# Kernel tuning notes

Hardware: AMD Instinct MI355X
Metric: run time of the kernel (lower is better)

## Reference

```python
import jax, jax.numpy as jnp
import numpy as np

B, D, S = 16, 512, 1500   # batch, input_size, seq_len
E, K, L = 8, 1024, 8      # embedding_size, num_embeddings, num_layers
TAU = 1.0
EPS = 1e-12               # F.normalize default eps


def setup_inputs() -> dict:
    key = jax.random.key(0)
    ks = jax.random.split(key, 5)
    x = jax.random.normal(ks[0], (B, D, S), dtype=jnp.float32)
    # weight-norm parametrized 1x1 conv params (v direction, g magnitude, bias)
    in_v = jax.random.normal(ks[1], (L, E, D), dtype=jnp.float32) * 0.05
    in_g = jnp.ones((L, E), dtype=jnp.float32)
    in_b = jnp.zeros((L, E), dtype=jnp.float32)
    out_v = jax.random.normal(ks[2], (L, D, E), dtype=jnp.float32) * 0.05
    out_g = jnp.ones((L, D), dtype=jnp.float32)
    out_b = jnp.zeros((L, D), dtype=jnp.float32)
    codebook = jax.random.normal(ks[3], (L, K, E), dtype=jnp.float32)
    return dict(x=x, in_v=in_v, in_g=in_g, in_b=in_b,
                out_v=out_v, out_g=out_g, out_b=out_b, codebook=codebook)


def _wn(v, g):
    # torch weight_norm (dim=0): w = g * v / ||v|| with norm over all dims except out-channel
    n = jnp.sqrt(jnp.sum(v * v, axis=1, keepdims=True))
    return g[:, None] * v / n


def _l2norm(x):
    # F.normalize(p=2, eps=1e-12)
    n = jnp.linalg.norm(x, axis=-1, keepdims=True)
    return x / jnp.maximum(n, EPS)


def _vq_layer(xr, iv, ig, ib, ov, og, ob, cb):
    Wi = _wn(iv, ig)                                              # [E, D]
    x_proj = jnp.einsum('ed,bds->bes', Wi, xr) + ib[:, None]      # [B, E, S]
    xf = x_proj.transpose(0, 2, 1).reshape(B * S, E)              # [B*S, E]
    xn = _l2norm(xf)
    cn = _l2norm(cb)                                              # [K, E]
    dist = (jnp.sum(xn * xn, axis=1, keepdims=True)
            - 2.0 * (xn @ cn.T)
            + jnp.sum(cn * cn, axis=1)[None, :])                  # [B*S, K]
    logits = -dist / TAU
    idxs = jnp.argmax(-dist, axis=1).reshape(B, S)                # [B, S]
    xq = cb[idxs].transpose(0, 2, 1)                              # [B, E, S] (un-normalized codebook)
    commit = jnp.mean((x_proj - jax.lax.stop_gradient(xq)) ** 2, axis=(1, 2))  # per-batch
    cbloss = jnp.mean((xq - jax.lax.stop_gradient(x_proj)) ** 2, axis=(1, 2))
    xq_st = x_proj + jax.lax.stop_gradient(xq - x_proj)           # straight-through
    Wo = _wn(ov, og)                                              # [D, E]
    xq_out = jnp.einsum('de,bes->bds', Wo, xq_st) + ob[:, None]   # [B, D, S]
    return xq_out, logits, idxs, commit, cbloss


def reference(x, in_v, in_g, in_b, out_v, out_g, out_b, codebook):
    # eval mode: all layers active, mask all-ones => masked mean == plain batch mean
    xq_sum = jnp.zeros_like(x)
    xr = x
    idxs_l, logits_l = [], []
    commit = jnp.float32(0.0)
    cbl = jnp.float32(0.0)
    for i in range(L):
        xq, lg, ix, cl, bl = _vq_layer(xr, in_v[i], in_g[i], in_b[i],
                                       out_v[i], out_g[i], out_b[i], codebook[i])
        xq_sum = xq_sum + xq
        xr = xr - xq
        commit = commit + jnp.mean(cl)
        cbl = cbl + jnp.mean(bl)
        idxs_l.append(ix)
        logits_l.append(lg)
    x_idxs = jnp.stack(idxs_l, axis=1)     # [B, L, S]
    x_logits = jnp.stack(logits_l, axis=1) # [B*S, L, K]
    return xq_sum, x_idxs, x_logits, commit, cbl
```

## Files before the change

### kernel.cpp

```cpp
#include <hip/hip_runtime.h>

constexpr int Lx = 8;
constexpr int Bx = 16;
constexpr int Dx = 512;
constexpr int Sx = 1500;
constexpr int Ex = 8;
constexpr int Kx = 1024;
constexpr int BS = Bx * Sx;
#define EPSF 1e-12f

__global__ __launch_bounds__(64) void k_wn_in(const float* __restrict__ v,
                                              const float* __restrict__ g,
                                              float* __restrict__ Wi) {
    int row = blockIdx.x;
    int lane = threadIdx.x;
    const float* vr = v + row * Dx;
    float s = 0.f;
    for (int j = lane; j < Dx; j += 64) { float t = vr[j]; s += t * t; }
    for (int off = 32; off; off >>= 1) s += __shfl_down(s, off);
    s = __shfl(s, 0);
    float scale = g[row] / sqrtf(s);
    for (int j = lane; j < Dx; j += 64) Wi[row * Dx + j] = vr[j] * scale;
}

__global__ __launch_bounds__(256) void k_wn_out_cb(const float* __restrict__ ov,
                                                   const float* __restrict__ og,
                                                   const float* __restrict__ cb,
                                                   float* __restrict__ Wo,
                                                   float* __restrict__ cn,
                                                   float* __restrict__ cc) {
    int r = blockIdx.x * blockDim.x + threadIdx.x;
    if (r < Lx * Dx) {
        const float* vr = ov + r * Ex;
        float s = 0.f;
        for (int e = 0; e < Ex; e++) s += vr[e] * vr[e];
        float sc = og[r] / sqrtf(s);
        for (int e = 0; e < Ex; e++) Wo[r * Ex + e] = vr[e] * sc;
    } else {
        int q = r - Lx * Dx;
        if (q < Lx * Kx) {
            const float* vr = cb + q * Ex;
            float s = 0.f;
            for (int e = 0; e < Ex; e++) s += vr[e] * vr[e];
            float n = fmaxf(sqrtf(s), EPSF);
            float s2 = 0.f, qv[Ex];
            for (int e = 0; e < Ex; e++) { qv[e] = vr[e] / n; s2 += qv[e] * qv[e]; }
            for (int e = 0; e < Ex; e++) cn[q * Ex + e] = qv[e];
            cc[q] = s2;
        }
    }
}


__global__ __launch_bounds__(256) void k_copyx(const float4* __restrict__ x,
                                               float4* __restrict__ xr,
                                               double* __restrict__ acc, unsigned n4) {
    unsigned i = blockIdx.x * blockDim.x + threadIdx.x;
    if (i == 0) *acc = 0.0;
    for (; i < n4; i += gridDim.x * blockDim.x) xr[i] = x[i];
}

__global__ __launch_bounds__(256) void k_proj(const float* __restrict__ xr,
                                              const float* __restrict__ Wi,
                                              const float* __restrict__ ib,
                                              float* __restrict__ xproj, int l) {
    __shared__ float wi[Ex * Dx];
    __shared__ float red[4 * Ex * 64];
    const float* W = Wi + l * Ex * Dx;
    for (int i = threadIdx.x; i < Ex * Dx; i += 256) wi[i] = W[i];
    __syncthreads();
    int col = threadIdx.x & 63;
    int grp = threadIdx.x >> 6;
    int c = blockIdx.x * 64 + col;
    int b = c / Sx, s = c % Sx;
    const float* xrb = xr + (size_t)b * Dx * Sx + s;
    float acc[Ex] = {0, 0, 0, 0, 0, 0, 0, 0};
    for (int d = grp * 128; d < grp * 128 + 128; d++) {
        float v = xrb[(size_t)d * Sx];
        #pragma unroll
        for (int e = 0; e < Ex; e++) acc[e] += wi[e * Dx + d] * v;
    }
    #pragma unroll
    for (int e = 0; e < Ex; e++) red[(grp * Ex + e) * 64 + col] = acc[e];
    __syncthreads();
    for (int o = threadIdx.x; o < Ex * 64; o += 256) {
        int e = o >> 6, cl = o & 63;
        float sum = red[(0 * Ex + e) * 64 + cl] + red[(1 * Ex + e) * 64 + cl] +
                    red[(2 * Ex + e) * 64 + cl] + red[(3 * Ex + e) * 64 + cl];
        int c2 = blockIdx.x * 64 + cl;
        int b2 = c2 / Sx, s2 = c2 % Sx;
        xproj[((size_t)b2 * Ex + e) * Sx + s2] = sum + ib[l * Ex + e];
    }
}

__global__ __launch_bounds__(256) void k_vq(const float* __restrict__ xproj,
                                            const float* __restrict__ cn,
                                            const float* __restrict__ cc,
                                            const float* __restrict__ cb,
                                            float* __restrict__ logits,
                                            float* __restrict__ idxs,
                                            float* __restrict__ xq,
                                            double* __restrict__ acc, int l) {
    __shared__ float4 cnt4[Kx * 2];
    __shared__ float  ccs[Kx];
    __shared__ float  bred[4];
    const float4* cn4 = (const float4*)(cn + (size_t)l * Kx * Ex);
    for (int i = threadIdx.x; i < Kx * 2; i += 256)
        cnt4[i ^ ((i >> 3) & 1)] = cn4[i];
    for (int i = threadIdx.x; i < Kx; i += 256) ccs[i] = cc[l * Kx + i];
    __syncthreads();
    int wave = threadIdx.x >> 6, lane = threadIdx.x & 63;
    float lossp = 0.f;
    for (int rr = 0; rr < 4; rr++) {
        int c = blockIdx.x * 16 + wave * 4 + rr;
        int b = c / Sx, s = c % Sx;
        float xp[Ex]; float xx2 = 0.f;
        #pragma unroll
        for (int e = 0; e < Ex; e++) {
            xp[e] = xproj[((size_t)b * Ex + e) * Sx + s];
            xx2 += xp[e] * xp[e];
        }
        float nrm = fmaxf(sqrtf(xx2), EPSF);
        float xn[Ex]; float xx = 0.f;
        #pragma unroll
        for (int e = 0; e < Ex; e++) { xn[e] = xp[e] / nrm; xx += xn[e] * xn[e]; }
        float* lrow = logits + ((size_t)c * Lx + l) * Kx;
        float best = -3.0e38f; int bk = 0;
        for (int j = 0; j < 16; j++) {
            int k = j * 64 + lane;
            float4 c0 = cnt4[(k * 2 + 0) ^ ((k >> 2) & 1)];
            float4 c1 = cnt4[(k * 2 + 1) ^ ((k >> 2) & 1)];
            float dot = xn[0] * c0.x + xn[1] * c0.y + xn[2] * c0.z + xn[3] * c0.w +
                        xn[4] * c1.x + xn[5] * c1.y + xn[6] * c1.z + xn[7] * c1.w;
            float lg = -(xx - 2.f * dot + ccs[k]);
            lrow[k] = lg;
            if (lg > best) { best = lg; bk = k; }
        }
        for (int off = 32; off; off >>= 1) {
            float ov = __shfl_xor(best, off);
            int   oi = __shfl_xor(bk, off);
            if (ov > best || (ov == best && oi < bk)) { best = ov; bk = oi; }
        }
        if (lane == 0) idxs[((size_t)b * Lx + l) * Sx + s] = (float)bk;
        const float* cbe = cb + ((size_t)l * Kx + bk) * Ex;
        if (lane < Ex) {
            float q = cbe[lane];
            xq[((size_t)b * Ex + lane) * Sx + s] = q;
            float dl = xp[lane] - q;
            lossp += dl * dl;
        }
    }
    for (int off = 32; off; off >>= 1) lossp += __shfl_down(lossp, off);
    if (lane == 0) bred[wave] = lossp;
    __syncthreads();
    if (threadIdx.x == 0) {
        float t = bred[0] + bred[1] + bred[2] + bred[3];
        atomicAdd(acc, (double)t);
    }
}

__global__ __launch_bounds__(256) void k_outproj(float* __restrict__ xr,
                                                 const float* __restrict__ xq,
                                                 const float* __restrict__ Wo,
                                                 const float* __restrict__ ob, int l) {
    const float* W   = Wo + l * Dx * Ex;
    const float* obl = ob + l * Dx;
    const unsigned S4 = Sx / 4;
    const unsigned n4 = Bx * Dx * S4;
    for (unsigned i = blockIdx.x * blockDim.x + threadIdx.x; i < n4;
         i += gridDim.x * blockDim.x) {
        unsigned s4 = i % S4;
        unsigned bd = i / S4;
        unsigned d = bd % Dx;
        unsigned b = bd / Dx;
        float4 av = {0, 0, 0, 0};
        #pragma unroll
        for (int e = 0; e < Ex; e++) {
            float w = W[d * Ex + e];
            float4 q = *(const float4*)(xq + ((size_t)b * Ex + e) * Sx + s4 * 4);
            av.x += w * q.x; av.y += w * q.y; av.z += w * q.z; av.w += w * q.w;
        }
        float bias = obl[d];
        float4 r = *(const float4*)(xr + (size_t)bd * Sx + s4 * 4);
        r.x -= av.x + bias; r.y -= av.y + bias;
        r.z -= av.z + bias; r.w -= av.w + bias;
        *(float4*)(xr + (size_t)bd * Sx + s4 * 4) = r;
    }
}

__global__ __launch_bounds__(256) void k_final(const float4* __restrict__ x,
                                               float4* __restrict__ out0,
                                               const double* __restrict__ acc,
                                               float* __restrict__ commit,
                                               float* __restrict__ cbl, unsigned n4) {
    unsigned i = blockIdx.x * blockDim.x + threadIdx.x;
    if (i == 0) {
        float v = (float)(*acc / (double)(Bx * Ex * Sx));
        *commit = v;
        *cbl = v;
    }
    for (; i < n4; i += gridDim.x * blockDim.x) {
        float4 a = x[i], b = out0[i];
        float4 o = {a.x - b.x, a.y - b.y, a.z - b.z, a.w - b.w};
        out0[i] = o;
    }
}

extern "C" void kernel_launch(void* const* d_in, const int* in_sizes, int n_in,
                              void* d_out, int out_size, void* d_ws, size_t ws_size,
                              hipStream_t stream) {
    const float* x     = (const float*)d_in[0];
    const float* in_v  = (const float*)d_in[1];
    const float* in_g  = (const float*)d_in[2];
    const float* in_b  = (const float*)d_in[3];
    const float* out_v = (const float*)d_in[4];
    const float* out_g = (const float*)d_in[5];
    const float* out_b = (const float*)d_in[6];
    const float* cb    = (const float*)d_in[7];

    float* out = (float*)d_out;
    float* xr       = out;
    float* oidx     = out + 12288000;
    float* ologits  = out + 12480000;
    float* ocommit  = out + 209088000;
    float* ocbl     = out + 209088001;

    char* w = (char*)d_ws;
    float*  Wi    = (float*)(w);
    float*  Wo    = (float*)(w + 131072);
    float*  cn    = (float*)(w + 262144);
    float*  cc    = (float*)(w + 524288);
    float*  xproj = (float*)(w + 557056);
    float*  xq    = (float*)(w + 1325056);
    double* acc   = (double*)(w + 2093056);

    k_wn_in<<<Lx * Ex, 64, 0, stream>>>(in_v, in_g, Wi);
    k_wn_out_cb<<<(Lx * Dx + Lx * Kx) / 256, 256, 0, stream>>>(out_v, out_g, cb, Wo, cn, cc);
    k_copyx<<<2048, 256, 0, stream>>>((const float4*)x, (float4*)xr, acc, 3072000u);

    for (int l = 0; l < Lx; l++) {
        k_proj<<<BS / 64, 256, 0, stream>>>(xr, Wi, in_b, xproj, l);
        k_vq<<<BS / 16, 256, 0, stream>>>(xproj, cn, cc, cb, ologits, oidx, xq, acc, l);
        k_outproj<<<2048, 256, 0, stream>>>(xr, xq, Wo, out_b, l);
    }
    k_final<<<2048, 256, 0, stream>>>((const float4*)x, (float4*)xr, acc,
                                      ocommit, ocbl, 3072000u);
}
```

Measured before the change: 760.8 us.

## Fuse all VQ layers into one register-resident megakernel per column tile

Replaces the per-layer projection, VQ and output-projection kernels with a single kernel in which each block holds 32 sequence columns of the residual (512 channels) in registers across all 8 layers. The residual is never written back to global memory between layers, which removes the repeated full-tensor reads and writes along with the copy and final kernels. The input weights are transposed so they can be read as float4. Holding 64 floats of residual per thread raises register pressure and the grid is smaller (750 blocks). The logits write stays the dominant traffic.

```diff
diff --git a/kernel.cpp b/kernel.cpp
--- a/kernel.cpp
+++ b/kernel.cpp
@@ -11,8 +11,9 @@
 
 __global__ __launch_bounds__(64) void k_wn_in(const float* __restrict__ v,
                                               const float* __restrict__ g,
-                                              float* __restrict__ Wi) {
+                                              float* __restrict__ WiT) {
     int row = blockIdx.x;
+    int l = row >> 3, e = row & 7;
     int lane = threadIdx.x;
     const float* vr = v + row * Dx;
     float s = 0.f;
@@ -20,7 +21,8 @@
     for (int off = 32; off; off >>= 1) s += __shfl_down(s, off);
     s = __shfl(s, 0);
     float scale = g[row] / sqrtf(s);
-    for (int j = lane; j < Dx; j += 64) Wi[row * Dx + j] = vr[j] * scale;
+    for (int j = lane; j < Dx; j += 64)
+        WiT[((size_t)l * Dx + j) * Ex + e] = vr[j] * scale;
 }
 
 __global__ __launch_bounds__(256) void k_wn_out_cb(const float* __restrict__ ov,
@@ -28,181 +30,180 @@
                                                    const float* __restrict__ cb,
                                                    float* __restrict__ Wo,
                                                    float* __restrict__ cn,
-                                                   float* __restrict__ cc) {
+                                                   float* __restrict__ cc,
+                                                   double* __restrict__ acc) {
     int r = blockIdx.x * blockDim.x + threadIdx.x;
+    if (r == 0) *acc = 0.0;
     if (r < Lx * Dx) {
         const float* vr = ov + r * Ex;
         float s = 0.f;
+        #pragma unroll
         for (int e = 0; e < Ex; e++) s += vr[e] * vr[e];
         float sc = og[r] / sqrtf(s);
+        #pragma unroll
         for (int e = 0; e < Ex; e++) Wo[r * Ex + e] = vr[e] * sc;
     } else {
         int q = r - Lx * Dx;
         if (q < Lx * Kx) {
             const float* vr = cb + q * Ex;
             float s = 0.f;
+            #pragma unroll
             for (int e = 0; e < Ex; e++) s += vr[e] * vr[e];
             float n = fmaxf(sqrtf(s), EPSF);
             float s2 = 0.f, qv[Ex];
+            #pragma unroll
             for (int e = 0; e < Ex; e++) { qv[e] = vr[e] / n; s2 += qv[e] * qv[e]; }
+            #pragma unroll
             for (int e = 0; e < Ex; e++) cn[q * Ex + e] = qv[e];
             cc[q] = s2;
         }
     }
 }
 
-
-__global__ __launch_bounds__(256) void k_copyx(const float4* __restrict__ x,
-                                               float4* __restrict__ xr,
-                                               double* __restrict__ acc, unsigned n4) {
-    unsigned i = blockIdx.x * blockDim.x + threadIdx.x;
-    if (i == 0) *acc = 0.0;
-    for (; i < n4; i += gridDim.x * blockDim.x) xr[i] = x[i];
-}
-
-__global__ __launch_bounds__(256) void k_proj(const float* __restrict__ xr,
-                                              const float* __restrict__ Wi,
-                                              const float* __restrict__ ib,
-                                              float* __restrict__ xproj, int l) {
-    __shared__ float wi[Ex * Dx];
-    __shared__ float red[4 * Ex * 64];
-    const float* W = Wi + l * Ex * Dx;
-    for (int i = threadIdx.x; i < Ex * Dx; i += 256) wi[i] = W[i];
-    __syncthreads();
-    int col = threadIdx.x & 63;
-    int grp = threadIdx.x >> 6;
-    int c = blockIdx.x * 64 + col;
-    int b = c / Sx, s = c % Sx;
-    const float* xrb = xr + (size_t)b * Dx * Sx + s;
-    float acc[Ex] = {0, 0, 0, 0, 0, 0, 0, 0};
-    for (int d = grp * 128; d < grp * 128 + 128; d++) {
-        float v = xrb[(size_t)d * Sx];
-        #pragma unroll
-        for (int e = 0; e < Ex; e++) acc[e] += wi[e * Dx + d] * v;
-    }
-    #pragma unroll
-    for (int e = 0; e < Ex; e++) red[(grp * Ex + e) * 64 + col] = acc[e];
-    __syncthreads();
-    for (int o = threadIdx.x; o < Ex * 64; o += 256) {
-        int e = o >> 6, cl = o & 63;
-        float sum = red[(0 * Ex + e) * 64 + cl] + red[(1 * Ex + e) * 64 + cl] +
-                    red[(2 * Ex + e) * 64 + cl] + red[(3 * Ex + e) * 64 + cl];
-        int c2 = blockIdx.x * 64 + cl;
-        int b2 = c2 / Sx, s2 = c2 % Sx;
-        xproj[((size_t)b2 * Ex + e) * Sx + s2] = sum + ib[l * Ex + e];
-    }
-}
-
-__global__ __launch_bounds__(256) void k_vq(const float* __restrict__ xproj,
-                                            const float* __restrict__ cn,
-                                            const float* __restrict__ cc,
-                                            const float* __restrict__ cb,
-                                            float* __restrict__ logits,
-                                            float* __restrict__ idxs,
-                                            float* __restrict__ xq,
-                                            double* __restrict__ acc, int l) {
+__global__ __launch_bounds__(256, 2) void k_mega(const float* __restrict__ x,
+                                                 const float* __restrict__ WiT,
+                                                 const float* __restrict__ ibias,
+                                                 const float* __restrict__ Wo,
+                                                 const float* __restrict__ obias,
+                                                 const float* __restrict__ cb,
+                                                 const float* __restrict__ cn,
+                                                 const float* __restrict__ cc,
+                                                 float* __restrict__ out0,
+                                                 float* __restrict__ oidx,
+                                                 float* __restrict__ logits,
+                                                 double* __restrict__ acc) {
     __shared__ float4 cnt4[Kx * 2];
     __shared__ float  ccs[Kx];
+    __shared__ float  red[8 * Ex * 32];
+    __shared__ float  xprojs[Ex * 32];
+    __shared__ float  xqs[Ex * 32];
     __shared__ float  bred[4];
-    const float4* cn4 = (const float4*)(cn + (size_t)l * Kx * Ex);
-    for (int i = threadIdx.x; i < Kx * 2; i += 256)
-        cnt4[i ^ ((i >> 3) & 1)] = cn4[i];
-    for (int i = threadIdx.x; i < Kx; i += 256) ccs[i] = cc[l * Kx + i];
-    __syncthreads();
-    int wave = threadIdx.x >> 6, lane = threadIdx.x & 63;
+
+    const int t = threadIdx.x;
+    const int col = t & 31;
+    const int g = t >> 5;
+    const int wave = t >> 6, lane = t & 63;
+    const int c = blockIdx.x * 32 + col;
+    const int b = c / Sx;
+    const int s = c - b * Sx;
+    const float* xcol = x + (size_t)b * Dx * Sx + s;
+
+    float xr[64];
+    #pragma unroll
+    for (int i = 0; i < 64; i++) xr[i] = xcol[(size_t)(g * 64 + i) * Sx];
+
     float lossp = 0.f;
-    for (int rr = 0; rr < 4; rr++) {
-        int c = blockIdx.x * 16 + wave * 4 + rr;
-        int b = c / Sx, s = c % Sx;
-        float xp[Ex]; float xx2 = 0.f;
-        #pragma unroll
-        for (int e = 0; e < Ex; e++) {
-            xp[e] = xproj[((size_t)b * Ex + e) * Sx + s];
-            xx2 += xp[e] * xp[e];
-        }
-        float nrm = fmaxf(sqrtf(xx2), EPSF);
-        float xn[Ex]; float xx = 0.f;
-        #pragma unroll
-        for (int e = 0; e < Ex; e++) { xn[e] = xp[e] / nrm; xx += xn[e] * xn[e]; }
-        float* lrow = logits + ((size_t)c * Lx + l) * Kx;
-        float best = -3.0e38f; int bk = 0;
-        for (int j = 0; j < 16; j++) {
-            int k = j * 64 + lane;
-            float4 c0 = cnt4[(k * 2 + 0) ^ ((k >> 2) & 1)];
-            float4 c1 = cnt4[(k * 2 + 1) ^ ((k >> 2) & 1)];
-            float dot = xn[0] * c0.x + xn[1] * c0.y + xn[2] * c0.z + xn[3] * c0.w +
-                        xn[4] * c1.x + xn[5] * c1.y + xn[6] * c1.z + xn[7] * c1.w;
-            float lg = -(xx - 2.f * dot + ccs[k]);
-            lrow[k] = lg;
-            if (lg > best) { best = lg; bk = k; }
-        }
-        for (int off = 32; off; off >>= 1) {
-            float ov = __shfl_xor(best, off);
-            int   oi = __shfl_xor(bk, off);
-            if (ov > best || (ov == best && oi < bk)) { best = ov; bk = oi; }
-        }
-        if (lane == 0) idxs[((size_t)b * Lx + l) * Sx + s] = (float)bk;
-        const float* cbe = cb + ((size_t)l * Kx + bk) * Ex;
-        if (lane < Ex) {
-            float q = cbe[lane];
-            xq[((size_t)b * Ex + lane) * Sx + s] = q;
-            float dl = xp[lane] - q;
-            lossp += dl * dl;
-        }
-    }
+
+    for (int l = 0; l < Lx; l++) {
+        const float4* cn4 = (const float4*)(cn + (size_t)l * Kx * Ex);
+        for (int i2 = t; i2 < Kx * 2; i2 += 256)
+            cnt4[i2 ^ ((i2 >> 3) & 1)] = cn4[i2];
+        for (int i2 = t; i2 < Kx; i2 += 256) ccs[i2] = cc[l * Kx + i2];
+        __syncthreads();
+
+        const float4* wt = (const float4*)(WiT + (size_t)l * Dx * Ex);
+        float pacc[8] = {0, 0, 0, 0, 0, 0, 0, 0};
+        #pragma unroll
+        for (int i = 0; i < 64; i++) {
+            int d = g * 64 + i;
+            float4 w0 = wt[d * 2 + 0];
+            float4 w1 = wt[d * 2 + 1];
+            float v = xr[i];
+            pacc[0] += w0.x * v; pacc[1] += w0.y * v;
+            pacc[2] += w0.z * v; pacc[3] += w0.w * v;
+            pacc[4] += w1.x * v; pacc[5] += w1.y * v;
+            pacc[6] += w1.z * v; pacc[7] += w1.w * v;
+        }
+        #pragma unroll
+        for (int e = 0; e < 8; e++) red[(g * 8 + e) * 32 + col] = pacc[e];
+        __syncthreads();
+
+        {
+            float sum = 0.f;
+            #pragma unroll
+            for (int gg = 0; gg < 8; gg++) sum += red[(gg * 8 + g) * 32 + col];
+            xprojs[g * 32 + col] = sum + ibias[l * Ex + g];
+        }
+        __syncthreads();
+
+        for (int cl = 0; cl < 8; cl++) {
+            int mycol = wave * 8 + cl;
+            int mc = blockIdx.x * 32 + mycol;
+            int mb = mc / Sx, ms = mc - mb * Sx;
+            float xp[8]; float xx2 = 0.f;
+            #pragma unroll
+            for (int e = 0; e < 8; e++) {
+                xp[e] = xprojs[e * 32 + mycol];
+                xx2 += xp[e] * xp[e];
+            }
+            float nrm = fmaxf(sqrtf(xx2), EPSF);
+            float xn[8]; float xx = 0.f;
+            #pragma unroll
+            for (int e = 0; e < 8; e++) { xn[e] = xp[e] / nrm; xx += xn[e] * xn[e]; }
+            float* lrow = logits + ((size_t)mc * Lx + l) * Kx;
+            float best = -3.0e38f; int bk = 0;
+            for (int j = 0; j < 16; j++) {
+                int k = j * 64 + lane;
+                float4 c0 = cnt4[(k * 2 + 0) ^ ((k >> 2) & 1)];
+                float4 c1 = cnt4[(k * 2 + 1) ^ ((k >> 2) & 1)];
+                float dot = xn[0] * c0.x + xn[1] * c0.y + xn[2] * c0.z + xn[3] * c0.w +
+                            xn[4] * c1.x + xn[5] * c1.y + xn[6] * c1.z + xn[7] * c1.w;
+                float lg = -(xx - 2.f * dot + ccs[k]);
+                lrow[k] = lg;
+                if (lg > best) { best = lg; bk = k; }
+            }
+            for (int off = 32; off; off >>= 1) {
+                float ov = __shfl_xor(best, off);
+                int   oi = __shfl_xor(bk, off);
+                if (ov > best || (ov == best && oi < bk)) { best = ov; bk = oi; }
+            }
+            if (lane == 0) oidx[((size_t)mb * Lx + l) * Sx + ms] = (float)bk;
+            if (lane < 8) {
+                float q = cb[((size_t)l * Kx + bk) * Ex + lane];
+                xqs[lane * 32 + mycol] = q;
+                float dl = xprojs[lane * 32 + mycol] - q;
+                lossp += dl * dl;
+            }
+        }
+        __syncthreads();
+
+        float xq[8];
+        #pragma unroll
+        for (int e = 0; e < 8; e++) xq[e] = xqs[e * 32 + col];
+        const float4* wo4 = (const float4*)(Wo + (size_t)l * Dx * Ex);
+        const float* obl = obias + l * Dx;
+        #pragma unroll
+        for (int i = 0; i < 64; i++) {
+            int d = g * 64 + i;
+            float4 w0 = wo4[d * 2 + 0];
+            float4 w1 = wo4[d * 2 + 1];
+            float dsum = w0.x * xq[0] + w0.y * xq[1] + w0.z * xq[2] + w0.w * xq[3] +
+                         w1.x * xq[4] + w1.y * xq[5] + w1.z * xq[6] + w1.w * xq[7] +
+                         obl[d];
+            xr[i] -= dsum;
+        }
+    }
+
+    float* ocol = out0 + (size_t)b * Dx * Sx + s;
+    #pragma unroll
+    for (int i = 0; i < 64; i++) {
+        float xv = xcol[(size_t)(g * 64 + i) * Sx];
+        ocol[(size_t)(g * 64 + i) * Sx] = xv - xr[i];
+    }
+
     for (int off = 32; off; off >>= 1) lossp += __shfl_down(lossp, off);
     if (lane == 0) bred[wave] = lossp;
     __syncthreads();
+    if (t == 0)
+        atomicAdd(acc, (double)(bred[0] + bred[1] + bred[2] + bred[3]));
+}
+
+__global__ void k_scalar(const double* __restrict__ acc,
+                         float* __restrict__ commit, float* __restrict__ cbl) {
     if (threadIdx.x == 0) {
-        float t = bred[0] + bred[1] + bred[2] + bred[3];
-        atomicAdd(acc, (double)t);
-    }
-}
-
-__global__ __launch_bounds__(256) void k_outproj(float* __restrict__ xr,
-                                                 const float* __restrict__ xq,
-                                                 const float* __restrict__ Wo,
-                                                 const float* __restrict__ ob, int l) {
-    const float* W   = Wo + l * Dx * Ex;
-    const float* obl = ob + l * Dx;
-    const unsigned S4 = Sx / 4;
-    const unsigned n4 = Bx * Dx * S4;
-    for (unsigned i = blockIdx.x * blockDim.x + threadIdx.x; i < n4;
-         i += gridDim.x * blockDim.x) {
-        unsigned s4 = i % S4;
-        unsigned bd = i / S4;
-        unsigned d = bd % Dx;
-        unsigned b = bd / Dx;
-        float4 av = {0, 0, 0, 0};
-        #pragma unroll
-        for (int e = 0; e < Ex; e++) {
-            float w = W[d * Ex + e];
-            float4 q = *(const float4*)(xq + ((size_t)b * Ex + e) * Sx + s4 * 4);
-            av.x += w * q.x; av.y += w * q.y; av.z += w * q.z; av.w += w * q.w;
-        }
-        float bias = obl[d];
-        float4 r = *(const float4*)(xr + (size_t)bd * Sx + s4 * 4);
-        r.x -= av.x + bias; r.y -= av.y + bias;
-        r.z -= av.z + bias; r.w -= av.w + bias;
-        *(float4*)(xr + (size_t)bd * Sx + s4 * 4) = r;
-    }
-}
-
-__global__ __launch_bounds__(256) void k_final(const float4* __restrict__ x,
-                                               float4* __restrict__ out0,
-                                               const double* __restrict__ acc,
-                                               float* __restrict__ commit,
-                                               float* __restrict__ cbl, unsigned n4) {
-    unsigned i = blockIdx.x * blockDim.x + threadIdx.x;
-    if (i == 0) {
-        float v = (float)(*acc / (double)(Bx * Ex * Sx));
+        float v = (float)(*acc / (double)((size_t)Bx * Ex * Sx));
         *commit = v;
         *cbl = v;
-    }
-    for (; i < n4; i += gridDim.x * blockDim.x) {
-        float4 a = x[i], b = out0[i];
-        float4 o = {a.x - b.x, a.y - b.y, a.z - b.z, a.w - b.w};
-        out0[i] = o;
     }
 }
 
@@ -219,30 +220,23 @@
     const float* cb    = (const float*)d_in[7];
 
     float* out = (float*)d_out;
-    float* xr       = out;
+    float* out0     = out;
     float* oidx     = out + 12288000;
     float* ologits  = out + 12480000;
     float* ocommit  = out + 209088000;
     float* ocbl     = out + 209088001;
 
     char* w = (char*)d_ws;
-    float*  Wi    = (float*)(w);
+    float*  WiT   = (float*)(w);
     float*  Wo    = (float*)(w + 131072);
     float*  cn    = (float*)(w + 262144);
     float*  cc    = (float*)(w + 524288);
-    float*  xproj = (float*)(w + 557056);
-    float*  xq    = (float*)(w + 1325056);
-    double* acc   = (double*)(w + 2093056);
-
-    k_wn_in<<<Lx * Ex, 64, 0, stream>>>(in_v, in_g, Wi);
-    k_wn_out_cb<<<(Lx * Dx + Lx * Kx) / 256, 256, 0, stream>>>(out_v, out_g, cb, Wo, cn, cc);
-    k_copyx<<<2048, 256, 0, stream>>>((const float4*)x, (float4*)xr, acc, 3072000u);
-
-    for (int l = 0; l < Lx; l++) {
-        k_proj<<<BS / 64, 256, 0, stream>>>(xr, Wi, in_b, xproj, l);
-        k_vq<<<BS / 16, 256, 0, stream>>>(xproj, cn, cc, cb, ologits, oidx, xq, acc, l);
-        k_outproj<<<2048, 256, 0, stream>>>(xr, xq, Wo, out_b, l);
-    }
-    k_final<<<2048, 256, 0, stream>>>((const float4*)x, (float4*)xr, acc,
-                                      ocommit, ocbl, 3072000u);
-}
+    double* acc   = (double*)(w + 557056);
+
+    k_wn_in<<<Lx * Ex, 64, 0, stream>>>(in_v, in_g, WiT);
+    k_wn_out_cb<<<(Lx * Dx + Lx * Kx) / 256, 256, 0, stream>>>(out_v, out_g, cb,
+                                                               Wo, cn, cc, acc);
+    k_mega<<<BS / 32, 256, 0, stream>>>(x, WiT, in_b, Wo, out_b, cb, cn, cc,
+                                        out0, oidx, ologits, acc);
+    k_scalar<<<1, 64, 0, stream>>>(acc, ocommit, ocbl);
+}
```

New measurement: 887.8 us. 1.17x slower.
